# Kernel optimization log

Measured on AMD Instinct MI355X. Metric: run time of the kernel, lower is better.

## Reference

```python
import math
import jax, jax.numpy as jnp
import numpy as np

B, S, D, H = 4, 2048, 1024, 16
DK = D // H
THETA = 10000.0


def _rope(xh, pos):
    # xh: [B, H, S, DK], pos: [S]
    half = jnp.arange(0, DK, 2, dtype=jnp.float32) / DK
    inv_freq = THETA ** (-half)                      # [DK/2]
    ang = pos.astype(jnp.float32)[:, None] * inv_freq  # [S, DK/2]
    cos, sin = jnp.cos(ang).astype(xh.dtype), jnp.sin(ang).astype(xh.dtype)
    x1, x2 = xh[..., 0::2], xh[..., 1::2]
    r1 = x1 * cos - x2 * sin
    r2 = x1 * sin + x2 * cos
    return jnp.stack([r1, r2], axis=-1).reshape(xh.shape)


def setup_inputs() -> dict:
    key = jax.random.key(0)
    kx, kq, kk, kv, ko = jax.random.split(key, 5)
    std = 0.02
    x = jax.random.normal(kx, (B, S, D), jnp.float32)
    wq = jax.random.normal(kq, (D, D), jnp.float32) * std
    wk = jax.random.normal(kk, (D, D), jnp.float32) * std
    wv = jax.random.normal(kv, (D, D), jnp.float32) * std
    wo = jax.random.normal(ko, (D, D), jnp.float32) * std
    token_positions = jnp.arange(S, dtype=jnp.int32)
    return {"x": x, "wq": wq, "wk": wk, "wv": wv, "wo": wo,
            "token_positions": token_positions}


def reference(x, wq, wk, wv, wo, token_positions):
    # bias-free linear projections: y = x @ W^T (torch Linear convention)
    q = x @ wq.T
    k = x @ wk.T
    v = x @ wv.T
    # split heads: [B, S, D] -> [B, H, S, DK]
    to_heads = lambda t: t.reshape(B, S, H, DK).transpose(0, 2, 1, 3)
    qh, kh, vh = to_heads(q), to_heads(k), to_heads(v)
    qh = _rope(qh, token_positions)
    kh = _rope(kh, token_positions)
    scores = jnp.einsum('bhqd,bhkd->bhqk', qh, kh) / math.sqrt(DK)
    causal = jnp.tril(jnp.ones((S, S), dtype=bool))
    scores = jnp.where(causal, scores, -jnp.inf)
    attn = jax.nn.softmax(scores, axis=-1)
    out = jnp.einsum('bhqk,bhkd->bhqd', attn, vh)       # [B, H, S, DK]
    out = out.transpose(0, 2, 1, 3).reshape(B, S, D)    # merge heads
    return out @ wo.T
```

## Files before the change

### kernel.cpp

```cpp
#include <hip/hip_runtime.h>

#define B_ 4
#define S_ 2048
#define D_ 1024
#define H_ 16
#define DK_ 64
#define M_ (B_*S_)
#define K_ D_
#define N_ D_

typedef unsigned short u16;
typedef unsigned int u32;
typedef __bf16 bf16x8 __attribute__((ext_vector_type(8)));
typedef float f32x4 __attribute__((ext_vector_type(4)));

__device__ __forceinline__ u16 f2bf(float f) {
    u32 u = __builtin_bit_cast(u32, f);
    u += 0x7fff + ((u >> 16) & 1);
    return (u16)(u >> 16);
}
__device__ __forceinline__ float bf2f(u16 h) {
    u32 u = ((u32)h) << 16;
    return __builtin_bit_cast(float, u);
}
__device__ __forceinline__ u32 pack_trunc(float a, float b) {
    return (__builtin_bit_cast(u32, a) >> 16) | (__builtin_bit_cast(u32, b) & 0xffff0000u);
}

#define GLDS16(g, l) __builtin_amdgcn_global_load_lds( \
    (__attribute__((address_space(1))) void*)(g),      \
    (__attribute__((address_space(3))) void*)(l), 16, 0, 0)

__global__ __launch_bounds__(256) void cvt_x(const float* __restrict__ in,
                                             u16* __restrict__ out, int n4) {
    const int i = blockIdx.x * 256 + threadIdx.x;
    if (i >= n4) return;
    const float4 f = *(const float4*)(in + (size_t)i * 4);
    u32 p0 = (u32)f2bf(f.x) | ((u32)f2bf(f.y) << 16);
    u32 p1 = (u32)f2bf(f.z) | ((u32)f2bf(f.w) << 16);
    *(uint2*)(out + (size_t)i * 4) = make_uint2(p0, p1);
}

__global__ __launch_bounds__(256) void cvt_w4(
    const float* __restrict__ w0, const float* __restrict__ w1,
    const float* __restrict__ w2, const float* __restrict__ w3,
    u16* __restrict__ o0, u16* __restrict__ o1,
    u16* __restrict__ o2, u16* __restrict__ o3) {
    const int wi = blockIdx.y;
    const float* in = (wi == 0) ? w0 : (wi == 1) ? w1 : (wi == 2) ? w2 : w3;
    u16* out       = (wi == 0) ? o0 : (wi == 1) ? o1 : (wi == 2) ? o2 : o3;
    const int i = blockIdx.x * 256 + threadIdx.x;
    const float4 f = *(const float4*)(in + (size_t)i * 4);
    u32 p0 = (u32)f2bf(f.x) | ((u32)f2bf(f.y) << 16);
    u32 p1 = (u32)f2bf(f.z) | ((u32)f2bf(f.w) << 16);
    *(uint2*)(out + (size_t)i * 4) = make_uint2(p0, p1);
}

template <int MODE>
__device__ __forceinline__ void gemm_tile(const u16* __restrict__ A,
                                          const u16* __restrict__ Bm,
                                          void* __restrict__ Cv) {
    __shared__ u16 As[128 * 32];
    __shared__ u16 Bs[128 * 32];
    const int tid  = threadIdx.x;
    const int wave = tid >> 6, lane = tid & 63;
    const int m0 = blockIdx.y * 128, n0 = blockIdx.x * 128;
    const int wm = wave & 1, wn = wave >> 1;
    const int quad = lane >> 4, mcol = lane & 15;

    const int c0 = wave, c1 = wave + 4;
    const int r0 = c0 * 16 + (lane >> 2), r1 = c1 * 16 + (lane >> 2);
    const int kb = (lane & 3) * 8;
    const u16* ga0 = A  + (size_t)(m0 + r0) * K_ + kb;
    const u16* ga1 = A  + (size_t)(m0 + r1) * K_ + kb;
    const u16* gb0 = Bm + (size_t)(n0 + r0) * K_ + kb;
    const u16* gb1 = Bm + (size_t)(n0 + r1) * K_ + kb;
    u16* la0 = &As[c0 * 512];
    u16* la1 = &As[c1 * 512];
    u16* lb0 = &Bs[c0 * 512];
    u16* lb1 = &Bs[c1 * 512];

    f32x4 acc[4][4];
#pragma unroll
    for (int i = 0; i < 4; i++)
#pragma unroll
        for (int j = 0; j < 4; j++) acc[i][j] = f32x4{0.f, 0.f, 0.f, 0.f};

    for (int kt = 0; kt < K_; kt += 32) {
        __syncthreads();
        GLDS16(ga0, la0); GLDS16(ga1, la1);
        GLDS16(gb0, lb0); GLDS16(gb1, lb1);
        ga0 += 32; ga1 += 32; gb0 += 32; gb1 += 32;
        __syncthreads();

        bf16x8 af[4], bfr[4];
#pragma unroll
        for (int i = 0; i < 4; i++) {
            af[i]  = *(const bf16x8*)&As[(size_t)(wm * 64 + i * 16 + mcol) * 32 + quad * 8];
            bfr[i] = *(const bf16x8*)&Bs[(size_t)(wn * 64 + i * 16 + mcol) * 32 + quad * 8];
        }
#pragma unroll
        for (int i = 0; i < 4; i++)
#pragma unroll
            for (int j = 0; j < 4; j++)
                acc[i][j] = __builtin_amdgcn_mfma_f32_16x16x32_bf16(
                    af[i], bfr[j], acc[i][j], 0, 0, 0);
    }

#pragma unroll
    for (int i = 0; i < 4; i++) {
        const int row = m0 + wm * 64 + i * 16 + quad * 4;
#pragma unroll
        for (int j = 0; j < 4; j++) {
            const int col = n0 + wn * 64 + j * 16 + mcol;
            if constexpr (MODE == 2) {
                const int hh = col >> 6, dd = col & 63;
                const int bb = row >> 11, ss = row & 2047;
                const u32 lo = (u32)f2bf(acc[i][j][0]) | ((u32)f2bf(acc[i][j][1]) << 16);
                const u32 hi = (u32)f2bf(acc[i][j][2]) | ((u32)f2bf(acc[i][j][3]) << 16);
                *(uint2*)((u16*)Cv + ((size_t)((bb * H_ + hh) * DK_ + dd)) * S_ + ss) =
                    make_uint2(lo, hi);
            } else {
#pragma unroll
                for (int r = 0; r < 4; r++) {
                    if constexpr (MODE == 1)
                        ((float*)Cv)[(size_t)(row + r) * N_ + col] = acc[i][j][r];
                    else
                        ((u16*)Cv)[(size_t)(row + r) * N_ + col] = f2bf(acc[i][j][r]);
                }
            }
        }
    }
}

__global__ __launch_bounds__(256) void gemm_qk_kernel(
    const u16* __restrict__ x,
    const u16* __restrict__ wq, const u16* __restrict__ wk,
    u16* __restrict__ q, u16* __restrict__ k) {
    const u16* Bm = (blockIdx.z == 0) ? wq : wk;
    u16* C        = (blockIdx.z == 0) ? q  : k;
    gemm_tile<0>(x, Bm, C);
}

__global__ __launch_bounds__(256) void gemm_v_kernel(
    const u16* __restrict__ x, const u16* __restrict__ wv, u16* __restrict__ vt) {
    gemm_tile<2>(x, wv, vt);
}

__global__ __launch_bounds__(256) void gemm_out_kernel(
    const u16* __restrict__ o, const u16* __restrict__ wo, float* __restrict__ out) {
    gemm_tile<1>(o, wo, out);
}

__global__ __launch_bounds__(256) void rope_qk(u16* __restrict__ q,
                                               u16* __restrict__ k,
                                               const int* __restrict__ pos) {
    const int idx = blockIdx.x * 256 + threadIdx.x;
    const int i = idx & 31;
    const int h = (idx >> 5) & (H_ - 1);
    const int s = (idx >> 9) & (S_ - 1);
    const int b = idx >> 20;
    const float p = (float)pos[s];
    const float inv = exp2f((float)i * (-13.287712379549449f / 32.f));
    const float ang = p * inv;
    float sn, cs;
    __sincosf(ang, &sn, &cs);
    const float QSC = 0.125f;
    const size_t off = ((size_t)(b * S_ + s)) * D_ + h * DK_ + 2 * i;
    {
        float x1 = bf2f(q[off]), x2 = bf2f(q[off + 1]);
        q[off]     = f2bf((x1 * cs - x2 * sn) * QSC);
        q[off + 1] = f2bf((x1 * sn + x2 * cs) * QSC);
    }
    {
        float x1 = bf2f(k[off]), x2 = bf2f(k[off + 1]);
        k[off]     = f2bf(x1 * cs - x2 * sn);
        k[off + 1] = f2bf(x1 * sn + x2 * cs);
    }
}

__global__ __launch_bounds__(256) void attn_kernel(
    const u16* __restrict__ q, const u16* __restrict__ k,
    const u16* __restrict__ vt, u16* __restrict__ o) {
    __shared__ u16 Qs[128][72];
    __shared__ u16 Ks[64][72];
    __shared__ u16 Vs[64][72];

    const int tid = threadIdx.x, wave = tid >> 6, lane = tid & 63;
    const int flat = blockIdx.x;
    const int qt = flat >> 6;
    const int h = flat & (H_ - 1);
    const int b = (flat >> 4) & 3;
    const int q0 = qt * 128;
    const int quad = lane >> 4, mcol = lane & 15;

    {
        const int rr = tid >> 1, cc = (tid & 1) * 32;
        const u16* src = q + ((size_t)(b * S_ + q0 + rr)) * D_ + h * DK_ + cc;
        u16* dst = &Qs[rr][cc];
        *(uint4*)(dst)      = *(const uint4*)(src);
        *(uint4*)(dst + 8)  = *(const uint4*)(src + 8);
        *(uint4*)(dst + 16) = *(const uint4*)(src + 16);
        *(uint4*)(dst + 24) = *(const uint4*)(src + 24);
    }
    __syncthreads();
    bf16x8 qf[2][2];
#pragma unroll
    for (int g = 0; g < 2; g++) {
        qf[g][0] = *(const bf16x8*)&Qs[wave * 32 + g * 16 + mcol][quad * 8];
        qf[g][1] = *(const bf16x8*)&Qs[wave * 32 + g * 16 + mcol][32 + quad * 8];
    }
    u16* PsW = &Qs[wave * 32][0];

    float m[2] = {-1e30f, -1e30f}, l[2] = {0.f, 0.f};
    f32x4 oacc[2][4];
#pragma unroll
    for (int g = 0; g < 2; g++)
#pragma unroll
        for (int dn = 0; dn < 4; dn++) oacc[g][dn] = f32x4{0.f, 0.f, 0.f, 0.f};

    const int rr2 = tid >> 2, ch2 = (tid & 3) * 16;
    const u16* krow = k + ((size_t)(b * S_ + rr2)) * D_ + h * DK_ + ch2;
    const u16* vrow = vt + ((size_t)((b * H_ + h) * DK_ + rr2)) * S_ + ch2;
    const int wq0 = q0 + wave * 32;
    const int jmax = 2 * qt + 1;

    uint4 kr0 = *(const uint4*)(krow);
    uint4 kr1 = *(const uint4*)(krow + 8);
    uint4 vr0 = *(const uint4*)(vrow);
    uint4 vr1 = *(const uint4*)(vrow + 8);

    for (int j = 0; j <= jmax; j++) {
        __syncthreads();
        *(uint4*)&Ks[rr2][ch2]     = kr0;
        *(uint4*)&Ks[rr2][ch2 + 8] = kr1;
        *(uint4*)&Vs[rr2][ch2]     = vr0;
        *(uint4*)&Vs[rr2][ch2 + 8] = vr1;
        __syncthreads();

        if (j < jmax) {
            kr0 = *(const uint4*)(krow + (size_t)(j + 1) * 64 * D_);
            kr1 = *(const uint4*)(krow + (size_t)(j + 1) * 64 * D_ + 8);
            vr0 = *(const uint4*)(vrow + (j + 1) * 64);
            vr1 = *(const uint4*)(vrow + (j + 1) * 64 + 8);
        }

        if (j * 64 > wq0 + 31) continue;

        f32x4 st[2][4];
#pragma unroll
        for (int n = 0; n < 4; n++) {
            bf16x8 kf0 = *(const bf16x8*)&Ks[n * 16 + mcol][quad * 8];
            bf16x8 kf1 = *(const bf16x8*)&Ks[n * 16 + mcol][32 + quad * 8];
            f32x4 z0 = f32x4{0.f, 0.f, 0.f, 0.f};
            z0 = __builtin_amdgcn_mfma_f32_16x16x32_bf16(kf0, qf[0][0], z0, 0, 0, 0);
            z0 = __builtin_amdgcn_mfma_f32_16x16x32_bf16(kf1, qf[0][1], z0, 0, 0, 0);
            st[0][n] = z0;
            f32x4 z1 = f32x4{0.f, 0.f, 0.f, 0.f};
            z1 = __builtin_amdgcn_mfma_f32_16x16x32_bf16(kf0, qf[1][0], z1, 0, 0, 0);
            z1 = __builtin_amdgcn_mfma_f32_16x16x32_bf16(kf1, qf[1][1], z1, 0, 0, 0);
            st[1][n] = z1;
        }

        if (j * 64 + 63 > wq0) {
#pragma unroll
            for (int g = 0; g < 2; g++) {
                const int qg = wq0 + g * 16 + mcol;
#pragma unroll
                for (int n = 0; n < 4; n++)
#pragma unroll
                    for (int r = 0; r < 4; r++)
                        if (j * 64 + n * 16 + quad * 4 + r > qg) st[g][n][r] = -1e30f;
            }
        }

        float alphaT[2][4];
#pragma unroll
        for (int g = 0; g < 2; g++) {
            float mx = st[g][0][0];
#pragma unroll
            for (int n = 0; n < 4; n++)
#pragma unroll
                for (int r = 0; r < 4; r++) mx = fmaxf(mx, st[g][n][r]);
            mx = fmaxf(mx, __shfl_xor(mx, 16));
            mx = fmaxf(mx, __shfl_xor(mx, 32));
            const float mnew = fmaxf(m[g], mx);
            const float al = __expf(m[g] - mnew);
            float sum = 0.f;
#pragma unroll
            for (int n = 0; n < 4; n++)
#pragma unroll
                for (int r = 0; r < 4; r++) {
                    const float p = __expf(st[g][n][r] - mnew);
                    st[g][n][r] = p;
                    sum += p;
                }
            sum += __shfl_xor(sum, 16);
            sum += __shfl_xor(sum, 32);
            l[g] = l[g] * al + sum;
            m[g] = mnew;
#pragma unroll
            for (int r = 0; r < 4; r++) alphaT[g][r] = __shfl(al, quad * 4 + r);
#pragma unroll
            for (int n = 0; n < 4; n++) {
                const u32 lo = pack_trunc(st[g][n][0], st[g][n][1]);
                const u32 hi = pack_trunc(st[g][n][2], st[g][n][3]);
                *(uint2*)&PsW[(g * 16 + mcol) * 72 + n * 16 + quad * 4] = make_uint2(lo, hi);
            }
        }

#pragma unroll
        for (int g = 0; g < 2; g++)
#pragma unroll
            for (int dn = 0; dn < 4; dn++)
#pragma unroll
                for (int r = 0; r < 4; r++) oacc[g][dn][r] *= alphaT[g][r];

        bf16x8 pf[2][2];
#pragma unroll
        for (int g = 0; g < 2; g++) {
            pf[g][0] = *(const bf16x8*)&PsW[(g * 16 + mcol) * 72 + quad * 8];
            pf[g][1] = *(const bf16x8*)&PsW[(g * 16 + mcol) * 72 + 32 + quad * 8];
        }
#pragma unroll
        for (int dn = 0; dn < 4; dn++) {
            bf16x8 vf0 = *(const bf16x8*)&Vs[dn * 16 + mcol][quad * 8];
            bf16x8 vf1 = *(const bf16x8*)&Vs[dn * 16 + mcol][32 + quad * 8];
#pragma unroll
            for (int g = 0; g < 2; g++) {
                oacc[g][dn] = __builtin_amdgcn_mfma_f32_16x16x32_bf16(pf[g][0], vf0, oacc[g][dn], 0, 0, 0);
                oacc[g][dn] = __builtin_amdgcn_mfma_f32_16x16x32_bf16(pf[g][1], vf1, oacc[g][dn], 0, 0, 0);
            }
        }
    }

#pragma unroll
    for (int g = 0; g < 2; g++) {
        float linv[4];
#pragma unroll
        for (int r = 0; r < 4; r++) linv[r] = 1.f / __shfl(l[g], quad * 4 + r);
#pragma unroll
        for (int dn = 0; dn < 4; dn++)
#pragma unroll
            for (int r = 0; r < 4; r++) {
                const int row = wq0 + g * 16 + quad * 4 + r;
                o[((size_t)(b * S_ + row)) * D_ + h * DK_ + dn * 16 + mcol] =
                    f2bf(oacc[g][dn][r] * linv[r]);
            }
    }
}

extern "C" void kernel_launch(void* const* d_in, const int* in_sizes, int n_in,
                              void* d_out, int out_size, void* d_ws, size_t ws_size,
                              hipStream_t stream) {
    const float* x  = (const float*)d_in[0];
    const float* wq = (const float*)d_in[1];
    const float* wk = (const float*)d_in[2];
    const float* wv = (const float*)d_in[3];
    const float* wo = (const float*)d_in[4];
    const int*   tp = (const int*)d_in[5];
    float* out = (float*)d_out;

    u16* ws = (u16*)d_ws;
    const size_t NE = (size_t)M_ * D_;
    const size_t WE = (size_t)N_ * K_;
    u16* xb  = ws;
    u16* wqb = ws + NE;
    u16* wkb = wqb + WE;
    u16* wvb = wkb + WE;
    u16* wob = wvb + WE;
    u16* qb  = wob + WE;
    u16* kb  = qb + NE;
    u16* vtb = (u16*)d_out;
    u16* ob  = xb;

    dim3 blk(256);
    cvt_x<<<dim3((int)(NE / 1024)), blk, 0, stream>>>(x, xb, (int)(NE / 4));
    cvt_w4<<<dim3((int)(WE / 1024), 4), blk, 0, stream>>>(wq, wk, wv, wo, wqb, wkb, wvb, wob);

    gemm_qk_kernel<<<dim3(N_ / 128, M_ / 128, 2), blk, 0, stream>>>(xb, wqb, wkb, qb, kb);
    gemm_v_kernel<<<dim3(N_ / 128, M_ / 128, 1), blk, 0, stream>>>(xb, wvb, vtb);
    rope_qk<<<dim3((B_ * S_ * H_ * 32) / 256), blk, 0, stream>>>(qb, kb, tp);
    attn_kernel<<<dim3((S_ / 128) * H_ * B_), blk, 0, stream>>>(qb, kb, vtb, ob);
    gemm_out_kernel<<<dim3(N_ / 128, M_ / 128, 1), blk, 0, stream>>>(ob, wob, out);
}
```

Before: 317.6 us.

## Keep softmax probabilities in registers via permuted K rows, use exp2 with lazy rescale

Permutes the order of K rows loaded into shared memory so the QK^T MFMA output layout lines up with the A-operand layout of the PV MFMA. The probabilities can then be packed straight from registers, with no round trip through shared memory and no Q staging buffer. Q fragments are loaded directly from global memory, and the log2(e) factor is folded into the Q scale so the softmax can use native exp2. The running max is only updated when it grows by more than 8 (in log2 units), which skips the alpha shuffle and accumulator rescale in most iterations. The risk is that a stale max allows values up to 2^8 before normalisation.

```diff
diff --git a/kernel.cpp b/kernel.cpp
--- a/kernel.cpp
+++ b/kernel.cpp
@@ -13,6 +13,9 @@
 typedef unsigned int u32;
 typedef __bf16 bf16x8 __attribute__((ext_vector_type(8)));
 typedef float f32x4 __attribute__((ext_vector_type(4)));
+typedef u32 u32x4v __attribute__((ext_vector_type(4)));
+
+#define EXP2F(x) __builtin_amdgcn_exp2f(x)
 
 __device__ __forceinline__ u16 f2bf(float f) {
     u32 u = __builtin_bit_cast(u32, f);
@@ -165,7 +168,7 @@
     const float ang = p * inv;
     float sn, cs;
     __sincosf(ang, &sn, &cs);
-    const float QSC = 0.125f;
+    const float QSC = 0.18033688011112042f;
     const size_t off = ((size_t)(b * S_ + s)) * D_ + h * DK_ + 2 * i;
     {
         float x1 = bf2f(q[off]), x2 = bf2f(q[off + 1]);
@@ -182,7 +185,6 @@
 __global__ __launch_bounds__(256) void attn_kernel(
     const u16* __restrict__ q, const u16* __restrict__ k,
     const u16* __restrict__ vt, u16* __restrict__ o) {
-    __shared__ u16 Qs[128][72];
     __shared__ u16 Ks[64][72];
     __shared__ u16 Vs[64][72];
 
@@ -193,24 +195,15 @@
     const int b = (flat >> 4) & 3;
     const int q0 = qt * 128;
     const int quad = lane >> 4, mcol = lane & 15;
-
-    {
-        const int rr = tid >> 1, cc = (tid & 1) * 32;
-        const u16* src = q + ((size_t)(b * S_ + q0 + rr)) * D_ + h * DK_ + cc;
-        u16* dst = &Qs[rr][cc];
-        *(uint4*)(dst)      = *(const uint4*)(src);
-        *(uint4*)(dst + 8)  = *(const uint4*)(src + 8);
-        *(uint4*)(dst + 16) = *(const uint4*)(src + 16);
-        *(uint4*)(dst + 24) = *(const uint4*)(src + 24);
-    }
-    __syncthreads();
+    const int wq0 = q0 + wave * 32;
+
     bf16x8 qf[2][2];
 #pragma unroll
     for (int g = 0; g < 2; g++) {
-        qf[g][0] = *(const bf16x8*)&Qs[wave * 32 + g * 16 + mcol][quad * 8];
-        qf[g][1] = *(const bf16x8*)&Qs[wave * 32 + g * 16 + mcol][32 + quad * 8];
-    }
-    u16* PsW = &Qs[wave * 32][0];
+        const u16* qs = q + ((size_t)(b * S_ + wq0 + g * 16 + mcol)) * D_ + h * DK_ + quad * 8;
+        qf[g][0] = *(const bf16x8*)qs;
+        qf[g][1] = *(const bf16x8*)(qs + 32);
+    }
 
     float m[2] = {-1e30f, -1e30f}, l[2] = {0.f, 0.f};
     f32x4 oacc[2][4];
@@ -220,9 +213,9 @@
         for (int dn = 0; dn < 4; dn++) oacc[g][dn] = f32x4{0.f, 0.f, 0.f, 0.f};
 
     const int rr2 = tid >> 2, ch2 = (tid & 3) * 16;
-    const u16* krow = k + ((size_t)(b * S_ + rr2)) * D_ + h * DK_ + ch2;
+    const int prr = (rr2 & 35) | ((rr2 & 12) << 1) | ((rr2 & 16) >> 2);
+    const u16* krow = k + ((size_t)(b * S_ + prr)) * D_ + h * DK_ + ch2;
     const u16* vrow = vt + ((size_t)((b * H_ + h) * DK_ + rr2)) * S_ + ch2;
-    const int wq0 = q0 + wave * 32;
     const int jmax = 2 * qt + 1;
 
     uint4 kr0 = *(const uint4*)(krow);
@@ -267,14 +260,15 @@
             for (int g = 0; g < 2; g++) {
                 const int qg = wq0 + g * 16 + mcol;
 #pragma unroll
-                for (int n = 0; n < 4; n++)
+                for (int n = 0; n < 4; n++) {
+                    const int tb = j * 64 + ((n >> 1) << 5) + ((n & 1) << 2) + quad * 8;
 #pragma unroll
                     for (int r = 0; r < 4; r++)
-                        if (j * 64 + n * 16 + quad * 4 + r > qg) st[g][n][r] = -1e30f;
-            }
-        }
-
-        float alphaT[2][4];
+                        if (tb + r > qg) st[g][n][r] = -1e30f;
+                }
+            }
+        }
+
 #pragma unroll
         for (int g = 0; g < 2; g++) {
             float mx = st[g][0][0];
@@ -284,44 +278,52 @@
                 for (int r = 0; r < 4; r++) mx = fmaxf(mx, st[g][n][r]);
             mx = fmaxf(mx, __shfl_xor(mx, 16));
             mx = fmaxf(mx, __shfl_xor(mx, 32));
-            const float mnew = fmaxf(m[g], mx);
-            const float al = __expf(m[g] - mnew);
+            float al = 1.f;
+            const bool need = !__all(mx <= m[g] + 8.f);
+            if (need) {
+                const float mnew = fmaxf(m[g], mx);
+                al = EXP2F(m[g] - mnew);
+                m[g] = mnew;
+            }
             float sum = 0.f;
 #pragma unroll
             for (int n = 0; n < 4; n++)
 #pragma unroll
                 for (int r = 0; r < 4; r++) {
-                    const float p = __expf(st[g][n][r] - mnew);
+                    const float p = EXP2F(st[g][n][r] - m[g]);
                     st[g][n][r] = p;
                     sum += p;
                 }
             sum += __shfl_xor(sum, 16);
             sum += __shfl_xor(sum, 32);
             l[g] = l[g] * al + sum;
-            m[g] = mnew;
-#pragma unroll
-            for (int r = 0; r < 4; r++) alphaT[g][r] = __shfl(al, quad * 4 + r);
-#pragma unroll
-            for (int n = 0; n < 4; n++) {
-                const u32 lo = pack_trunc(st[g][n][0], st[g][n][1]);
-                const u32 hi = pack_trunc(st[g][n][2], st[g][n][3]);
-                *(uint2*)&PsW[(g * 16 + mcol) * 72 + n * 16 + quad * 4] = make_uint2(lo, hi);
-            }
-        }
-
-#pragma unroll
-        for (int g = 0; g < 2; g++)
-#pragma unroll
-            for (int dn = 0; dn < 4; dn++)
-#pragma unroll
-                for (int r = 0; r < 4; r++) oacc[g][dn][r] *= alphaT[g][r];
+            if (need) {
+                float alphaT[4];
+#pragma unroll
+                for (int r = 0; r < 4; r++) alphaT[r] = __shfl(al, quad * 4 + r);
+#pragma unroll
+                for (int dn = 0; dn < 4; dn++)
+#pragma unroll
+                    for (int r = 0; r < 4; r++) oacc[g][dn][r] *= alphaT[r];
+            }
+        }
 
         bf16x8 pf[2][2];
 #pragma unroll
         for (int g = 0; g < 2; g++) {
-            pf[g][0] = *(const bf16x8*)&PsW[(g * 16 + mcol) * 72 + quad * 8];
-            pf[g][1] = *(const bf16x8*)&PsW[(g * 16 + mcol) * 72 + 32 + quad * 8];
-        }
+            u32x4v w0, w1;
+            w0[0] = pack_trunc(st[g][0][0], st[g][0][1]);
+            w0[1] = pack_trunc(st[g][0][2], st[g][0][3]);
+            w0[2] = pack_trunc(st[g][1][0], st[g][1][1]);
+            w0[3] = pack_trunc(st[g][1][2], st[g][1][3]);
+            w1[0] = pack_trunc(st[g][2][0], st[g][2][1]);
+            w1[1] = pack_trunc(st[g][2][2], st[g][2][3]);
+            w1[2] = pack_trunc(st[g][3][0], st[g][3][1]);
+            w1[3] = pack_trunc(st[g][3][2], st[g][3][3]);
+            pf[g][0] = __builtin_bit_cast(bf16x8, w0);
+            pf[g][1] = __builtin_bit_cast(bf16x8, w1);
+        }
+
 #pragma unroll
         for (int dn = 0; dn < 4; dn++) {
             bf16x8 vf0 = *(const bf16x8*)&Vs[dn * 16 + mcol][quad * 8];
```

Result: faster. 305.6 us (-3.8%).
